# Kernel optimization log

Hardware: AMD Instinct MI355X
Metric: run time of the kernel (lower is better)

## Reference

```python
import jax, jax.numpy as jnp
import numpy as np

N_THRESH = 100  # thresholds = 0.00, 0.01, ..., 0.99


def setup_inputs() -> dict:
    key = jax.random.key(0)
    k1, k2 = jax.random.split(key)
    predicted_mask = jax.random.uniform(k1, (32, 1, 1024, 1024), dtype=jnp.float32)
    gt_mask = jax.random.randint(k2, (32, 1, 1024, 1024), 0, 2, dtype=jnp.int32)
    return {"predicted_mask": predicted_mask, "gt_mask": gt_mask}


def reference(predicted_mask, gt_mask):
    # Single-pass histogram formulation of: for each t_k in arange(0,1,0.01),
    # iou_k = |(pred > t_k) & gt| / |(pred > t_k) | gt|  (torchmetrics binary Jaccard,
    # strict '>' thresholding, safe-divide -> 0 when union is empty).
    thresholds = jnp.arange(0.0, 1.0, 0.01, dtype=jnp.float32)  # [100], sorted
    pred = jnp.squeeze(predicted_mask).ravel()                  # [N] probabilities in [0,1]
    gt = jnp.squeeze(gt_mask).ravel().astype(jnp.float32)       # [N] 0/1

    # cnt[i] = number of thresholds strictly below pred[i]; pixel i satisfies
    # (pred > t_k) exactly for k in [0, cnt[i]).
    cnt = jnp.searchsorted(thresholds, pred, side='left')       # [N] int in [0, 100]

    hist_pos = jax.ops.segment_sum(gt, cnt, num_segments=N_THRESH + 1)              # [101]
    hist_all = jax.ops.segment_sum(jnp.ones_like(gt), cnt, num_segments=N_THRESH + 1)

    # TP_k = #{pred > t_k and gt==1} = sum_{c > k} hist_pos[c]  (suffix sums via cumsum)
    tp = jnp.sum(hist_pos) - jnp.cumsum(hist_pos)[:N_THRESH]        # [100]
    pred_pos = jnp.sum(hist_all) - jnp.cumsum(hist_all)[:N_THRESH]  # [100] #{pred > t_k}
    n_gt_pos = jnp.sum(gt)

    union = pred_pos + n_gt_pos - tp                                 # TP + FP + FN
    ious = jnp.where(union > 0, tp / jnp.maximum(union, 1.0), 0.0)   # safe divide -> 0
    return thresholds, ious
```

## Files before the change

kernel.cpp:

```cpp
#include <hip/hip_runtime.h>
#include <stdint.h>

#define N_THRESH 100
#define NBINS 101
#define NWORDS 51
#define STEP_ELEMS 1024
#define STEPS 16
#define TILE_ELEMS (STEP_ELEMS * STEPS)

typedef __attribute__((address_space(3))) uint32_t lds_u32_t;
typedef __attribute__((address_space(1))) uint32_t glob_u32_t;

__global__ void zero_ws_kernel(unsigned long long* __restrict__ ws) {
    int i = threadIdx.x;
    if (i < NBINS) ws[i] = 0ull;
}

__device__ __forceinline__ int bin_of(float v) {
    int e = (int)(v * 100.0f);
    e = e < 0 ? 0 : (e > 99 ? 99 : e);
    double ed = (double)e * 0.01;
    float t0 = (float)ed;
    float t1 = (float)(ed + 0.01);
    int c = e + (t0 < v ? 1 : 0) + (t1 < v ? 1 : 0);
    return c > N_THRESH ? N_THRESH : c;
}

__device__ __forceinline__ void stage(const float* __restrict__ pred,
                                      const int* __restrict__ gt,
                                      float* spb, int* sgb,
                                      int ebase, int wave, int lane) {
    const float* srcp = pred + ebase + wave * 256 + lane * 4;
    const int*   srcg = gt   + ebase + wave * 256 + lane * 4;
    __builtin_amdgcn_global_load_lds((glob_u32_t*)srcp,
                                     (lds_u32_t*)(spb + wave * 256), 16, 0, 0);
    __builtin_amdgcn_global_load_lds((glob_u32_t*)srcg,
                                     (lds_u32_t*)(sgb + wave * 256), 16, 0, 0);
}

__global__ __launch_bounds__(256) void hist_kernel(
        const float* __restrict__ pred,
        const int* __restrict__ gt,
        unsigned long long* __restrict__ ws,
        int n) {
    __shared__ uint32_t hist[4][NWORDS][64];
    __shared__ __align__(16) float sp[2][STEP_ELEMS];
    __shared__ __align__(16) int   sg[2][STEP_ELEMS];
    __shared__ uint32_t pcnt[NBINS], ppos[NBINS];

    const int tid  = threadIdx.x;
    const int wave = tid >> 6;
    const int lane = tid & 63;
    uint32_t* __restrict__ hw = &hist[wave][0][0];

    if (tid < NBINS) { pcnt[tid] = 0u; ppos[tid] = 0u; }

    const int tiles = (n + TILE_ELEMS - 1) / TILE_ELEMS;
    for (int t = blockIdx.x; t < tiles; t += gridDim.x) {
        const int base = t * TILE_ELEMS;
        for (int i = lane; i < NWORDS * 64; i += 64) hw[i] = 0u;
        __syncthreads();

        const int limit = (n - base < TILE_ELEMS) ? (n - base) : TILE_ELEMS;
        if (limit == TILE_ELEMS) {
            stage(pred, gt, sp[0], sg[0], base, wave, lane);
            __syncthreads();
            for (int s = 0; s < STEPS; ++s) {
                const int b = s & 1;
                if (s + 1 < STEPS)
                    stage(pred, gt, sp[b ^ 1], sg[b ^ 1],
                          base + (s + 1) * STEP_ELEMS, wave, lane);
                float4 p = ((const float4*)sp[b])[tid];
                int4   g = ((const int4*)sg[b])[tid];
                {
                    int c0 = bin_of(p.x), c1 = bin_of(p.y);
                    int c2 = bin_of(p.z), c3 = bin_of(p.w);
                    hist[wave][c0 >> 1][lane] +=
                        (1u | ((uint32_t)(g.x != 0) << 8)) << ((c0 & 1) * 16);
                    hist[wave][c1 >> 1][lane] +=
                        (1u | ((uint32_t)(g.y != 0) << 8)) << ((c1 & 1) * 16);
                    hist[wave][c2 >> 1][lane] +=
                        (1u | ((uint32_t)(g.z != 0) << 8)) << ((c2 & 1) * 16);
                    hist[wave][c3 >> 1][lane] +=
                        (1u | ((uint32_t)(g.w != 0) << 8)) << ((c3 & 1) * 16);
                }
                __syncthreads();
            }
        } else {
            for (int k = base + tid; k < base + limit; k += 256) {
                int c = bin_of(pred[k]);
                hist[wave][c >> 1][lane] +=
                    (1u | ((uint32_t)(gt[k] != 0) << 8)) << ((c & 1) * 16);
            }
            __syncthreads();
        }

        if (lane < NWORDS) {
            uint32_t c0 = 0, p0 = 0, c1 = 0, p1 = 0;
            for (int c = 0; c < 64; ++c) {
                uint32_t v = hist[wave][lane][(c + lane) & 63];
                c0 += v & 0xffu;         p0 += (v >> 8) & 0xffu;
                c1 += (v >> 16) & 0xffu; p1 += v >> 24;
            }
            const int b0 = lane * 2, b1 = lane * 2 + 1;
            atomicAdd(&pcnt[b0], c0);
            atomicAdd(&ppos[b0], p0);
            if (b1 < NBINS) {
                atomicAdd(&pcnt[b1], c1);
                atomicAdd(&ppos[b1], p1);
            }
        }
        __syncthreads();
    }

    if (tid < NBINS) {
        unsigned long long s =
            ((unsigned long long)ppos[tid] << 32) | (unsigned long long)pcnt[tid];
        if (s) atomicAdd(&ws[tid], s);
    }
}

__global__ void finalize_kernel(const unsigned long long* __restrict__ ws,
                                float* __restrict__ out) {
    __shared__ unsigned int pos[NBINS], all[NBINS];
    int k = threadIdx.x;
    if (k < NBINS) {
        unsigned long long h = ws[k];
        pos[k] = (unsigned int)(h >> 32);
        all[k] = (unsigned int)(h & 0xffffffffull);
    }
    __syncthreads();
    if (k < N_THRESH) {
        out[k] = (float)((double)k * 0.01);
        unsigned long long tp = 0, pp = 0, ngt = 0;
        for (int c = k + 1; c <= N_THRESH; ++c) { tp += pos[c]; pp += all[c]; }
        for (int c = 0; c <= N_THRESH; ++c) ngt += pos[c];
        long long uni = (long long)(pp + ngt - tp);
        double iou = (uni > 0) ? (double)tp / (double)uni : 0.0;
        out[N_THRESH + k] = (float)iou;
    }
}

extern "C" void kernel_launch(void* const* d_in, const int* in_sizes, int n_in,
                              void* d_out, int out_size, void* d_ws, size_t ws_size,
                              hipStream_t stream) {
    const float* pred = (const float*)d_in[0];
    const int*   gt   = (const int*)d_in[1];
    float* out = (float*)d_out;
    unsigned long long* ws = (unsigned long long*)d_ws;
    int n = in_sizes[0];

    zero_ws_kernel<<<1, 128, 0, stream>>>(ws);
    hist_kernel<<<512, 256, 0, stream>>>(pred, gt, ws, n);
    finalize_kernel<<<1, 128, 0, stream>>>(ws, out);
}
```

Measured before the change: 319.8 us.

## Replace LDS-staged tiled histogram with grid-stride register-prefetch single pass

Drops the async global-to-LDS double-buffered staging, which needed a block barrier every 1024 elements and a histogram flush per 16K-element tile. Each thread now walks a grid stride over float4/int4 vectors, prefetching the next pair into registers, and flushes its per-lane histogram only once at the end. The grid grows with n so no lane exceeds 200 elements, keeping the packed 8-bit counters from overflowing. The trade-off is less explicit latency hiding: only one vector is in flight per thread, and the odd tail is handled by a single thread.

```diff
diff --git a/kernel.cpp b/kernel.cpp
--- a/kernel.cpp
+++ b/kernel.cpp
@@ -4,12 +4,6 @@
 #define N_THRESH 100
 #define NBINS 101
 #define NWORDS 51
-#define STEP_ELEMS 1024
-#define STEPS 16
-#define TILE_ELEMS (STEP_ELEMS * STEPS)
-
-typedef __attribute__((address_space(3))) uint32_t lds_u32_t;
-typedef __attribute__((address_space(1))) uint32_t glob_u32_t;
 
 __global__ void zero_ws_kernel(unsigned long long* __restrict__ ws) {
     int i = threadIdx.x;
@@ -26,92 +20,82 @@
     return c > N_THRESH ? N_THRESH : c;
 }
 
-__device__ __forceinline__ void stage(const float* __restrict__ pred,
-                                      const int* __restrict__ gt,
-                                      float* spb, int* sgb,
-                                      int ebase, int wave, int lane) {
-    const float* srcp = pred + ebase + wave * 256 + lane * 4;
-    const int*   srcg = gt   + ebase + wave * 256 + lane * 4;
-    __builtin_amdgcn_global_load_lds((glob_u32_t*)srcp,
-                                     (lds_u32_t*)(spb + wave * 256), 16, 0, 0);
-    __builtin_amdgcn_global_load_lds((glob_u32_t*)srcg,
-                                     (lds_u32_t*)(sgb + wave * 256), 16, 0, 0);
-}
-
 __global__ __launch_bounds__(256) void hist_kernel(
         const float* __restrict__ pred,
         const int* __restrict__ gt,
         unsigned long long* __restrict__ ws,
         int n) {
     __shared__ uint32_t hist[4][NWORDS][64];
-    __shared__ __align__(16) float sp[2][STEP_ELEMS];
-    __shared__ __align__(16) int   sg[2][STEP_ELEMS];
     __shared__ uint32_t pcnt[NBINS], ppos[NBINS];
 
     const int tid  = threadIdx.x;
     const int wave = tid >> 6;
     const int lane = tid & 63;
-    uint32_t* __restrict__ hw = &hist[wave][0][0];
 
+    for (int i = lane; i < NWORDS * 64; i += 64) (&hist[wave][0][0])[i] = 0u;
     if (tid < NBINS) { pcnt[tid] = 0u; ppos[tid] = 0u; }
 
-    const int tiles = (n + TILE_ELEMS - 1) / TILE_ELEMS;
-    for (int t = blockIdx.x; t < tiles; t += gridDim.x) {
-        const int base = t * TILE_ELEMS;
-        for (int i = lane; i < NWORDS * 64; i += 64) hw[i] = 0u;
-        __syncthreads();
+    const int nvec = n >> 2;
+    const float4* __restrict__ p4 = (const float4*)pred;
+    const int4*   __restrict__ g4 = (const int4*)gt;
+    const int gsz = gridDim.x * blockDim.x;
 
-        const int limit = (n - base < TILE_ELEMS) ? (n - base) : TILE_ELEMS;
-        if (limit == TILE_ELEMS) {
-            stage(pred, gt, sp[0], sg[0], base, wave, lane);
-            __syncthreads();
-            for (int s = 0; s < STEPS; ++s) {
-                const int b = s & 1;
-                if (s + 1 < STEPS)
-                    stage(pred, gt, sp[b ^ 1], sg[b ^ 1],
-                          base + (s + 1) * STEP_ELEMS, wave, lane);
-                float4 p = ((const float4*)sp[b])[tid];
-                int4   g = ((const int4*)sg[b])[tid];
-                {
-                    int c0 = bin_of(p.x), c1 = bin_of(p.y);
-                    int c2 = bin_of(p.z), c3 = bin_of(p.w);
-                    hist[wave][c0 >> 1][lane] +=
-                        (1u | ((uint32_t)(g.x != 0) << 8)) << ((c0 & 1) * 16);
-                    hist[wave][c1 >> 1][lane] +=
-                        (1u | ((uint32_t)(g.y != 0) << 8)) << ((c1 & 1) * 16);
-                    hist[wave][c2 >> 1][lane] +=
-                        (1u | ((uint32_t)(g.z != 0) << 8)) << ((c2 & 1) * 16);
-                    hist[wave][c3 >> 1][lane] +=
-                        (1u | ((uint32_t)(g.w != 0) << 8)) << ((c3 & 1) * 16);
-                }
-                __syncthreads();
-            }
-        } else {
-            for (int k = base + tid; k < base + limit; k += 256) {
-                int c = bin_of(pred[k]);
-                hist[wave][c >> 1][lane] +=
-                    (1u | ((uint32_t)(gt[k] != 0) << 8)) << ((c & 1) * 16);
-            }
-            __syncthreads();
+    int i = blockIdx.x * blockDim.x + tid;
+    if (i < nvec) {
+        float4 p = p4[i];
+        int4   g = g4[i];
+        for (int j = i + gsz; j < nvec; j += gsz) {
+            float4 pn = p4[j];
+            int4   gn = g4[j];
+            int c0 = bin_of(p.x), c1 = bin_of(p.y);
+            int c2 = bin_of(p.z), c3 = bin_of(p.w);
+            hist[wave][c0 >> 1][lane] +=
+                (1u | ((uint32_t)(g.x != 0) << 8)) << ((c0 & 1) * 16);
+            hist[wave][c1 >> 1][lane] +=
+                (1u | ((uint32_t)(g.y != 0) << 8)) << ((c1 & 1) * 16);
+            hist[wave][c2 >> 1][lane] +=
+                (1u | ((uint32_t)(g.z != 0) << 8)) << ((c2 & 1) * 16);
+            hist[wave][c3 >> 1][lane] +=
+                (1u | ((uint32_t)(g.w != 0) << 8)) << ((c3 & 1) * 16);
+            p = pn; g = gn;
         }
+        int c0 = bin_of(p.x), c1 = bin_of(p.y);
+        int c2 = bin_of(p.z), c3 = bin_of(p.w);
+        hist[wave][c0 >> 1][lane] +=
+            (1u | ((uint32_t)(g.x != 0) << 8)) << ((c0 & 1) * 16);
+        hist[wave][c1 >> 1][lane] +=
+            (1u | ((uint32_t)(g.y != 0) << 8)) << ((c1 & 1) * 16);
+        hist[wave][c2 >> 1][lane] +=
+            (1u | ((uint32_t)(g.z != 0) << 8)) << ((c2 & 1) * 16);
+        hist[wave][c3 >> 1][lane] +=
+            (1u | ((uint32_t)(g.w != 0) << 8)) << ((c3 & 1) * 16);
+    }
 
-        if (lane < NWORDS) {
-            uint32_t c0 = 0, p0 = 0, c1 = 0, p1 = 0;
-            for (int c = 0; c < 64; ++c) {
-                uint32_t v = hist[wave][lane][(c + lane) & 63];
-                c0 += v & 0xffu;         p0 += (v >> 8) & 0xffu;
-                c1 += (v >> 16) & 0xffu; p1 += v >> 24;
-            }
-            const int b0 = lane * 2, b1 = lane * 2 + 1;
-            atomicAdd(&pcnt[b0], c0);
-            atomicAdd(&ppos[b0], p0);
-            if (b1 < NBINS) {
-                atomicAdd(&pcnt[b1], c1);
-                atomicAdd(&ppos[b1], p1);
-            }
+    if (blockIdx.x == 0 && tid == 0) {
+        for (int k = nvec << 2; k < n; ++k) {
+            int c = bin_of(pred[k]);
+            hist[0][c >> 1][0] +=
+                (1u | ((uint32_t)(gt[k] != 0) << 8)) << ((c & 1) * 16);
         }
-        __syncthreads();
     }
+
+    __syncthreads();
+    if (lane < NWORDS) {
+        uint32_t c0 = 0, p0 = 0, c1 = 0, p1 = 0;
+        for (int c = 0; c < 64; ++c) {
+            uint32_t v = hist[wave][lane][(c + lane) & 63];
+            c0 += v & 0xffu;         p0 += (v >> 8) & 0xffu;
+            c1 += (v >> 16) & 0xffu; p1 += v >> 24;
+        }
+        const int b0 = lane * 2, b1 = lane * 2 + 1;
+        atomicAdd(&pcnt[b0], c0);
+        atomicAdd(&ppos[b0], p0);
+        if (b1 < NBINS) {
+            atomicAdd(&pcnt[b1], c1);
+            atomicAdd(&ppos[b1], p1);
+        }
+    }
+    __syncthreads();
 
     if (tid < NBINS) {
         unsigned long long s =
@@ -151,6 +135,9 @@
     int n = in_sizes[0];
 
     zero_ws_kernel<<<1, 128, 0, stream>>>(ws);
-    hist_kernel<<<512, 256, 0, stream>>>(pred, gt, ws, n);
+    int grid = 768;
+    int need = (n + 51199) / 51200;
+    if (need > grid) grid = need;
+    hist_kernel<<<grid, 256, 0, stream>>>(pred, gt, ws, n);
     finalize_kernel<<<1, 128, 0, stream>>>(ws, out);
 }
```

Result: faster. 285.9 us (-10.6%).
